# Performance work log

Hardware: AMD Instinct MI355X
Metric: run time of the kernel (lower is better)

The kernel has to match this reference:

```python
import jax, jax.numpy as jnp
import numpy as np

B, S, HID, NH = 2, 2048, 2048, 16
DH = HID // NH  # 128


def _rope_tables(seq_len, dim, dtype=jnp.float32):
    inv_freq = 1.0 / (10000.0 ** (jnp.arange(0, dim, 2, dtype=jnp.float32) / dim))
    t = jnp.arange(seq_len, dtype=jnp.float32)
    freqs = jnp.einsum('i,j->ij', t, inv_freq)          # [S, dim/2]
    emb = jnp.concatenate([freqs, freqs], axis=-1)       # [S, dim]
    return jnp.cos(emb)[None, None].astype(dtype), jnp.sin(emb)[None, None].astype(dtype)


def _rotate_half(x):
    x1, x2 = x[..., : x.shape[-1] // 2], x[..., x.shape[-1] // 2 :]
    return jnp.concatenate([-x2, x1], axis=-1)


def setup_inputs() -> dict:
    key = jax.random.key(0)
    ks = jax.random.split(key, 6)
    hidden_states = jax.random.normal(ks[0], (B, S, HID), dtype=jnp.float32)
    scale = 1.0 / np.sqrt(HID)
    Wq = jax.random.normal(ks[1], (HID, HID), dtype=jnp.float32) * scale
    Wk = jax.random.normal(ks[2], (HID, HID), dtype=jnp.float32) * scale
    Wv = jax.random.normal(ks[3], (HID, HID), dtype=jnp.float32) * scale
    Wo = jax.random.normal(ks[4], (HID, HID), dtype=jnp.float32) * scale
    bq = jnp.zeros((HID,), jnp.float32)
    bk = jnp.zeros((HID,), jnp.float32)
    bv = jnp.zeros((HID,), jnp.float32)
    bo = jnp.zeros((HID,), jnp.float32)
    # causal additive mask [1,1,S,S]
    causal = jnp.tril(jnp.ones((S, S), dtype=bool))
    attention_mask = jnp.where(causal, 0.0, -1e9).astype(jnp.float32)[None, None]
    return dict(hidden_states=hidden_states, attention_mask=attention_mask,
                Wq=Wq, bq=bq, Wk=Wk, bk=bk, Wv=Wv, bv=bv, Wo=Wo, bo=bo)


def reference(hidden_states, attention_mask, Wq, bq, Wk, bk, Wv, bv, Wo, bo):
    b, s, _ = hidden_states.shape
    # torch Linear: x @ W.T + b
    q = (hidden_states @ Wq.T + bq).reshape(b, s, NH, DH).transpose(0, 2, 1, 3)
    k = (hidden_states @ Wk.T + bk).reshape(b, s, NH, DH).transpose(0, 2, 1, 3)
    v = (hidden_states @ Wv.T + bv).reshape(b, s, NH, DH).transpose(0, 2, 1, 3)
    cos, sin = _rope_tables(s, DH)
    q = q * cos + _rotate_half(q) * sin
    k = k * cos + _rotate_half(k) * sin
    scores = jnp.einsum('bhqd,bhkd->bhqk', q * (DH ** -0.5), k)
    scores = scores + attention_mask
    probs = jax.nn.softmax(scores, axis=-1)  # dropout: eval mode (identity)
    out = jnp.einsum('bhqk,bhkd->bhqd', probs, v)
    out = out.transpose(0, 2, 1, 3).reshape(b, s, HID)
    return out @ Wo.T + bo
```

## Files before the change

kernel.cpp:

```cpp
#include <hip/hip_runtime.h>
#include <hip/hip_bf16.h>
#include <cstdint>
#include <cstddef>

#define BB 2
#define SS 2048
#define HH 2048
#define NHH 16
#define DHH 128

using f32x4  = __attribute__((ext_vector_type(4))) float;
using bf16x8 = __attribute__((ext_vector_type(8))) __bf16;
using bf16x4 = __attribute__((ext_vector_type(4))) __bf16;
using bfloat = __bf16;

__device__ inline void gload_lds16(const void* g, void* l) {
    __builtin_amdgcn_global_load_lds(
        (const __attribute__((address_space(1))) void*)g,
        (__attribute__((address_space(3))) void*)l, 16, 0, 0);
}

__device__ inline f32x4 mfma16(bf16x8 a, bf16x8 b, f32x4 c) {
    return __builtin_amdgcn_mfma_f32_16x16x32_bf16(a, b, c, 0, 0, 0);
}

template <int CTRL>
__device__ inline float dpp_max_step(float x) {
    int y = __builtin_amdgcn_update_dpp(0, __builtin_bit_cast(int, x), CTRL, 0xf, 0xf, false);
    return fmaxf(x, __builtin_bit_cast(float, y));
}
__device__ inline float rowmax16(float x) {
    x = dpp_max_step<0x121>(x);
    x = dpp_max_step<0x122>(x);
    x = dpp_max_step<0x124>(x);
    x = dpp_max_step<0x128>(x);
    return x;
}

__global__ void prep_all(const float* __restrict__ hs,
                         const float* __restrict__ w0, const float* __restrict__ w1,
                         const float* __restrict__ w2, const float* __restrict__ w3,
                         bfloat* __restrict__ xb,
                         bfloat* __restrict__ d0, bfloat* __restrict__ d1,
                         bfloat* __restrict__ d2, bfloat* __restrict__ d3,
                         float* __restrict__ cosT, float* __restrict__ sinT) {
    const int bid = blockIdx.x, tid = threadIdx.x;
    if (bid < 8192 + 16384) {
        const float* s;
        bfloat* d;
        int i;
        if (bid < 8192) {
            s = hs; d = xb; i = bid * 256 + tid;
        } else {
            int b2 = bid - 8192, sel = b2 >> 12;
            s = sel == 0 ? w0 : sel == 1 ? w1 : sel == 2 ? w2 : w3;
            d = sel == 0 ? d0 : sel == 1 ? d1 : sel == 2 ? d2 : d3;
            i = (b2 & 4095) * 256 + tid;
        }
        float4 v = reinterpret_cast<const float4*>(s)[i];
        bf16x4 o;
        o[0] = (bfloat)v.x; o[1] = (bfloat)v.y; o[2] = (bfloat)v.z; o[3] = (bfloat)v.w;
        reinterpret_cast<bf16x4*>(d)[i] = o;
    } else {
        int i = (bid - 24576) * 256 + tid;
        int s = i >> 6, j = i & 63;
        float invf = powf(10000.0f, -(float)j / 64.0f);
        float ang = (float)s * invf;
        cosT[i] = cosf(ang);
        sinT[i] = sinf(ang);
    }
}

__device__ __forceinline__ void kloop128(const bfloat* __restrict__ Ag,
                                         const bfloat* __restrict__ Bg,
                                         f32x4 (&acc)[4][4]) {
    constexpr int K = HH, NT = K / 32;
    __shared__ bfloat As[2][128 * 32];
    __shared__ bfloat Bs[2][128 * 32];
    const int t = threadIdx.x, l = t & 63, lr = l & 15, lg = l >> 4;
    const int w = t >> 6, wm = (w >> 1) * 64, wc = w & 1;
    const int ubase = t & ~63;

    auto stage = [&](int buf, int kt) {
#pragma unroll
        for (int i = 0; i < 2; i++) {
            int idx = i * 256 + t;
            int r = idx >> 2, u = idx & 3;
            int us = u ^ (r & 3) ^ ((r >> 2) & 1);
            gload_lds16(Ag + (size_t)r * K + kt * 32 + us * 8,
                        &As[buf][(i * 256 + ubase) * 8]);
        }
#pragma unroll
        for (int i = 0; i < 2; i++) {
            int idx = i * 256 + t;
            int r = idx >> 2, u = idx & 3;
            int us = u ^ (r & 3) ^ ((r >> 2) & 1);
            gload_lds16(Bg + (size_t)r * K + kt * 32 + us * 8,
                        &Bs[buf][(i * 256 + ubase) * 8]);
        }
    };

    stage(0, 0);

#pragma unroll 1
    for (int kt = 0; kt < NT; ++kt) {
        const int buf = kt & 1;
        asm volatile("s_waitcnt vmcnt(0)" ::: "memory");
        __builtin_amdgcn_s_barrier();
        __builtin_amdgcn_sched_barrier(0);
        if (kt + 1 < NT) stage(buf ^ 1, kt + 1);

        const bfloat* A_ = As[buf];
        const bfloat* B_ = Bs[buf];
        bf16x8 af[4], bfr[4];
#pragma unroll
        for (int mi = 0; mi < 4; mi++) {
            int row = wm + mi * 16 + lr;
            int us = lg ^ (row & 3) ^ ((row >> 2) & 1);
            af[mi] = *reinterpret_cast<const bf16x8*>(&A_[row * 32 + us * 8]);
        }
#pragma unroll
        for (int ni = 0; ni < 4; ni++) {
            int row = wc * 32 + (ni & 1) * 16 + (ni >> 1) * 64 + lr;
            int us = lg ^ (row & 3) ^ ((row >> 2) & 1);
            bfr[ni] = *reinterpret_cast<const bf16x8*>(&B_[row * 32 + us * 8]);
        }
        __builtin_amdgcn_s_setprio(1);
#pragma unroll
        for (int mi = 0; mi < 4; mi++)
#pragma unroll
            for (int ni = 0; ni < 4; ni++)
                acc[mi][ni] = mfma16(af[mi], bfr[ni], acc[mi][ni]);
        __builtin_amdgcn_s_setprio(0);
        __builtin_amdgcn_sched_barrier(0);
    }
}

__global__ __launch_bounds__(256, 4)
void gemm_qkv(const bfloat* __restrict__ A,
              const bfloat* __restrict__ Bq, const bfloat* __restrict__ Bk,
              const bfloat* __restrict__ Bv,
              const float* __restrict__ bq, const float* __restrict__ bk,
              const float* __restrict__ bv,
              bfloat* __restrict__ Qo, bfloat* __restrict__ Ko, bfloat* __restrict__ Vto,
              const float* __restrict__ cosT, const float* __restrict__ sinT) {
    constexpr int K = HH, N = HH;
    const int sel = blockIdx.y >> 4;
    const bfloat* Bt = sel == 0 ? Bq : sel == 1 ? Bk : Bv;
    const float* bias = sel == 0 ? bq : sel == 1 ? bk : bv;
    const int m0 = blockIdx.x * 128, n0 = (blockIdx.y & 15) * 128;

    f32x4 acc[4][4] = {};
    kloop128(A + (size_t)m0 * K, Bt + (size_t)n0 * K, acc);

    const int t = threadIdx.x, l = t & 63, lr = l & 15, lg = l >> 4;
    const int w = t >> 6, wm = (w >> 1) * 64, wc = w & 1;

    if (sel == 2) {
#pragma unroll
        for (int mi = 0; mi < 4; mi++) {
            int row = m0 + wm + mi * 16 + lg * 4;
            int bb = row >> 11;
            int s0 = row & (SS - 1);
#pragma unroll
            for (int ni = 0; ni < 4; ni++) {
                int cb = wc * 32 + (ni & 1) * 16 + (ni >> 1) * 64;
                int col = n0 + cb + lr;
                float bv_ = bias[col];
                bf16x4 pack;
#pragma unroll
                for (int j = 0; j < 4; j++)
                    pack[j] = (bfloat)(acc[mi][ni][j] + bv_);
                *reinterpret_cast<bf16x4*>(
                    &Vto[((size_t)(bb * HH + col)) * SS + s0]) = pack;
            }
        }
    } else {
        bfloat* C = sel == 0 ? Qo : Ko;
        const float qs = sel == 0 ? 0.088388347648318447f : 1.0f;
#pragma unroll
        for (int mi = 0; mi < 4; mi++) {
            int row = m0 + wm + mi * 16 + lg * 4;
#pragma unroll
            for (int ni = 0; ni < 2; ni++) {
                int d = wc * 32 + ni * 16 + lr;
                int col1 = n0 + d, col2 = col1 + 64;
                float b1 = bias[col1], b2 = bias[col2];
#pragma unroll
                for (int j = 0; j < 4; j++) {
                    int r = row + j, s = r & (SS - 1);
                    float c  = cosT[s * 64 + d];
                    float sn = sinT[s * 64 + d];
                    float x1 = acc[mi][ni][j] + b1;
                    float x2 = acc[mi][ni + 2][j] + b2;
                    C[(size_t)r * N + col1] = (bfloat)((x1 * c - x2 * sn) * qs);
                    C[(size_t)r * N + col2] = (bfloat)((x2 * c + x1 * sn) * qs);
                }
            }
        }
    }
}

__global__ __launch_bounds__(256, 4)
void gemm_out(const bfloat* __restrict__ A, const bfloat* __restrict__ Bt,
              const float* __restrict__ bias, float* __restrict__ C) {
    constexpr int K = HH, N = HH;
    const int m0 = blockIdx.x * 128, n0 = blockIdx.y * 128;

    f32x4 acc[4][4] = {};
    kloop128(A + (size_t)m0 * K, Bt + (size_t)n0 * K, acc);

    const int t = threadIdx.x, l = t & 63, lr = l & 15, lg = l >> 4;
    const int w = t >> 6, wm = (w >> 1) * 64, wc = w & 1;
#pragma unroll
    for (int mi = 0; mi < 4; mi++) {
        int row = m0 + wm + mi * 16 + lg * 4;
#pragma unroll
        for (int ni = 0; ni < 4; ni++) {
            int cb = wc * 32 + (ni & 1) * 16 + (ni >> 1) * 64;
            int col = n0 + cb + lr;
            float bv = bias[col];
#pragma unroll
            for (int j = 0; j < 4; j++)
                C[(size_t)(row + j) * N + col] = acc[mi][ni][j] + bv;
        }
    }
}

__global__ __launch_bounds__(256, 4)
void attn_fwd(const bfloat* __restrict__ Q, const bfloat* __restrict__ K,
              const bfloat* __restrict__ Vt, bfloat* __restrict__ O) {
    __shared__ bfloat Ks[64 * 128];
    __shared__ bfloat Vs[128 * 64];
    __shared__ bfloat Pw[4][16 * 64];

    const int t = threadIdx.x, w = t >> 6, l = t & 63;
    const int lr = l & 15, lg = l >> 4;
    const int swz = (lr & 7) << 4;

    const int f = blockIdx.x;
    const int xcd = f & 7, slot = f >> 3;
    const int bh = xcd + 8 * (slot >> 5);
    const int qidx = 31 - (slot & 31);
    const int b = bh >> 4, h = bh & 15;
    const int q0 = qidx * 64 + w * 16;

    const size_t bo_ = (size_t)b * SS * HH + (size_t)h * DHH;
    const bfloat* Qp = Q + bo_;
    const bfloat* Kp = K + bo_;
    const bfloat* Vp = Vt + (size_t)(b * NHH + h) * DHH * SS;
    bfloat* Op = O + bo_;

    auto stage = [&](int kv0) {
#pragma unroll
        for (int i = 0; i < 4; i++) {
            int Ub = (i * 4 + w) * 64;
            int U = Ub + l;
            int r = U >> 4;
            int u = (U & 15) ^ (r & 7);
            gload_lds16(Kp + (size_t)(kv0 + r) * HH + u * 8, &Ks[Ub * 8]);
        }
#pragma unroll
        for (int i = 0; i < 4; i++) {
            int Ub = (i * 4 + w) * 64;
            int U = Ub + l;
            int r = U >> 3;
            int u = (U & 7) ^ (r & 7);
            gload_lds16(Vp + (size_t)r * SS + kv0 + u * 8, &Vs[Ub * 8]);
        }
    };

    bf16x8 qf[4];
#pragma unroll
    for (int kt = 0; kt < 4; kt++)
        qf[kt] = *reinterpret_cast<const bf16x8*>(Qp + (size_t)(q0 + lr) * HH + kt * 32 + lg * 8);

    bf16x8 ones;
#pragma unroll
    for (int e = 0; e < 8; e++) ones[e] = (bfloat)1.0f;

    f32x4 o[8] = {};
    f32x4 lsv = {};
    float m[4];
#pragma unroll
    for (int j = 0; j < 4; j++) m[j] = -1e30f;

    const int nkv = qidx + 1;

    for (int kv = 0; kv < nkv; ++kv) {
        stage(kv * 64);
        __syncthreads();

        const char* KB = (const char*)&Ks[0];
        const char* VB = (const char*)&Vs[0];

        f32x4 sc[4] = {};
        __builtin_amdgcn_s_setprio(1);
#pragma unroll
        for (int kt = 0; kt < 4; kt++) {
            const int col = (kt * 64 + lg * 16);
#pragma unroll
            for (int kb = 0; kb < 4; kb++) {
                bf16x8 kf = *reinterpret_cast<const bf16x8*>(
                    KB + (kb * 16 + lr) * 256 + (col ^ swz));
                sc[kb] = mfma16(qf[kt], kf, sc[kb]);
            }
        }
        __builtin_amdgcn_s_setprio(0);

        const bool diag = (kv == nkv - 1);
        float p[4][4], alpha[4];
        bool ga = false;
#pragma unroll
        for (int j = 0; j < 4; j++) {
            float v0 = sc[0][j], v1 = sc[1][j], v2 = sc[2][j], v3 = sc[3][j];
            if (diag) {
                int qr = q0 + lg * 4 + j;
                int k0 = kv * 64 + lr;
                if (k0      > qr) v0 = -1e30f;
                if (k0 + 16 > qr) v1 = -1e30f;
                if (k0 + 32 > qr) v2 = -1e30f;
                if (k0 + 48 > qr) v3 = -1e30f;
            }
            float mx = rowmax16(fmaxf(fmaxf(v0, v1), fmaxf(v2, v3)));
            bool grow = mx > m[j] + 8.0f;
            float mn = grow ? mx : m[j];
            alpha[j] = grow ? __expf(m[j] - mn) : 1.0f;
            m[j] = mn;
            ga = ga || grow;
            p[0][j] = __expf(v0 - mn);
            p[1][j] = __expf(v1 - mn);
            p[2][j] = __expf(v2 - mn);
            p[3][j] = __expf(v3 - mn);
        }
        if (__any(ga)) {
#pragma unroll
            for (int j = 0; j < 4; j++) {
                lsv[j] *= alpha[j];
#pragma unroll
                for (int nt = 0; nt < 8; nt++) o[nt][j] *= alpha[j];
            }
        }

        char* pwb = (char*)&Pw[w][0];
#pragma unroll
        for (int j = 0; j < 4; j++) {
            int q = lg * 4 + j;
            int qs = (q & 7) << 4;
#pragma unroll
            for (int kb = 0; kb < 4; kb++)
                *(bfloat*)(pwb + q * 128 + ((kb * 32 + lr * 2) ^ qs)) = (bfloat)p[kb][j];
        }
        asm volatile("s_waitcnt lgkmcnt(0)" ::: "memory");
        __builtin_amdgcn_sched_barrier(0);

        const char* pwr = (const char*)&Pw[w][0];
        bf16x8 pa0 = *reinterpret_cast<const bf16x8*>(pwr + lr * 128 + ((lg * 16) ^ swz));
        bf16x8 pa1 = *reinterpret_cast<const bf16x8*>(pwr + lr * 128 + ((64 + lg * 16) ^ swz));
        __builtin_amdgcn_s_setprio(1);
        lsv = mfma16(pa0, ones, lsv);
        lsv = mfma16(pa1, ones, lsv);
#pragma unroll
        for (int nt = 0; nt < 8; nt++) {
            const char* vb = VB + (nt * 16 + lr) * 128;
            bf16x8 vf0 = *reinterpret_cast<const bf16x8*>(vb + ((lg * 16) ^ swz));
            bf16x8 vf1 = *reinterpret_cast<const bf16x8*>(vb + ((64 + lg * 16) ^ swz));
            o[nt] = mfma16(pa0, vf0, o[nt]);
            o[nt] = mfma16(pa1, vf1, o[nt]);
        }
        __builtin_amdgcn_s_setprio(0);
        __syncthreads();
    }

#pragma unroll
    for (int j = 0; j < 4; j++) {
        float inv = 1.0f / lsv[j];
        int row = q0 + lg * 4 + j;
#pragma unroll
        for (int nt = 0; nt < 8; nt++)
            Op[(size_t)row * HH + nt * 16 + lr] = (bfloat)(o[nt][j] * inv);
    }
}

extern "C" void kernel_launch(void* const* d_in, const int* in_sizes, int n_in,
                              void* d_out, int out_size, void* d_ws, size_t ws_size,
                              hipStream_t stream) {
    (void)in_sizes; (void)n_in; (void)out_size; (void)ws_size;
    const float* hs = (const float*)d_in[0];
    const float* Wq = (const float*)d_in[2];
    const float* bq = (const float*)d_in[3];
    const float* Wk = (const float*)d_in[4];
    const float* bk = (const float*)d_in[5];
    const float* Wv = (const float*)d_in[6];
    const float* bv = (const float*)d_in[7];
    const float* Wo = (const float*)d_in[8];
    const float* bo = (const float*)d_in[9];

    char* ws = (char*)d_ws;
    size_t off = 0;
    auto alloc = [&](size_t bytes) { void* p = ws + off; off += (bytes + 255) & ~(size_t)255; return p; };
    const size_t MK = (size_t)BB * SS * HH;
    const size_t NK = (size_t)HH * HH;

    bfloat* Xb  = (bfloat*)alloc(MK * 2);
    bfloat* Wqb = (bfloat*)alloc(NK * 2);
    bfloat* Wkb = (bfloat*)alloc(NK * 2);
    bfloat* Wvb = (bfloat*)alloc(NK * 2);
    bfloat* Wob = (bfloat*)alloc(NK * 2);
    bfloat* Qb  = (bfloat*)alloc(MK * 2);
    bfloat* Kb  = (bfloat*)alloc(MK * 2);
    bfloat* Vtb = (bfloat*)alloc(MK * 2);
    float*  cosT = (float*)alloc((size_t)SS * 64 * 4);
    float*  sinT = (float*)alloc((size_t)SS * 64 * 4);
    bfloat* AOb = Xb;

    prep_all<<<8192 + 16384 + 512, 256, 0, stream>>>(
        hs, Wq, Wk, Wv, Wo, Xb, Wqb, Wkb, Wvb, Wob, cosT, sinT);

    gemm_qkv<<<dim3(32, 48), 256, 0, stream>>>(
        Xb, Wqb, Wkb, Wvb, bq, bk, bv, Qb, Kb, Vtb, cosT, sinT);

    attn_fwd<<<1024, 256, 0, stream>>>(Qb, Kb, Vtb, AOb);

    gemm_out<<<dim3(32, 16), 256, 0, stream>>>(AOb, Wob, bo, (float*)d_out);
}
```

Baseline: 307.6 us.

## Pair causal query tiles per block and double-buffer K/V staging in attention

Each attention block now handles two 64-row query tiles, qa and 31-qa, from the same head. This balances causal work across blocks, and each staged K/V tile serves both query tiles, halving the grid. K/V staging uses two LDS buffers, so the next tile's global-to-LDS load is issued before computing on the current one, replacing the per-iteration full sync pattern. The cost is more registers (two sets of accumulators and Q fragments) and double the LDS. Launch bounds drop from 4 to 2 blocks per CU, which reduces occupancy.

```diff
diff --git a/kernel.cpp b/kernel.cpp
--- a/kernel.cpp
+++ b/kernel.cpp
@@ -227,11 +227,11 @@
     }
 }
 
-__global__ __launch_bounds__(256, 4)
+__global__ __launch_bounds__(256, 2)
 void attn_fwd(const bfloat* __restrict__ Q, const bfloat* __restrict__ K,
               const bfloat* __restrict__ Vt, bfloat* __restrict__ O) {
-    __shared__ bfloat Ks[64 * 128];
-    __shared__ bfloat Vs[128 * 64];
+    __shared__ bfloat Ks[2][64 * 128];
+    __shared__ bfloat Vs[2][128 * 64];
     __shared__ bfloat Pw[4][16 * 64];
 
     const int t = threadIdx.x, w = t >> 6, l = t & 63;
@@ -239,11 +239,10 @@
     const int swz = (lr & 7) << 4;
 
     const int f = blockIdx.x;
-    const int xcd = f & 7, slot = f >> 3;
-    const int bh = xcd + 8 * (slot >> 5);
-    const int qidx = 31 - (slot & 31);
+    const int bh = f & 31, p = f >> 5;
+    const int qa = p, qb = 31 - p;
     const int b = bh >> 4, h = bh & 15;
-    const int q0 = qidx * 64 + w * 16;
+    const int q0a = qa * 64 + w * 16, q0b = qb * 64 + w * 16;
 
     const size_t bo_ = (size_t)b * SS * HH + (size_t)h * DHH;
     const bfloat* Qp = Q + bo_;
@@ -251,14 +250,14 @@
     const bfloat* Vp = Vt + (size_t)(b * NHH + h) * DHH * SS;
     bfloat* Op = O + bo_;
 
-    auto stage = [&](int kv0) {
+    auto stage = [&](int buf, int kv0) {
 #pragma unroll
         for (int i = 0; i < 4; i++) {
             int Ub = (i * 4 + w) * 64;
             int U = Ub + l;
             int r = U >> 4;
             int u = (U & 15) ^ (r & 7);
-            gload_lds16(Kp + (size_t)(kv0 + r) * HH + u * 8, &Ks[Ub * 8]);
+            gload_lds16(Kp + (size_t)(kv0 + r) * HH + u * 8, &Ks[buf][Ub * 8]);
         }
 #pragma unroll
         for (int i = 0; i < 4; i++) {
@@ -266,34 +265,29 @@
             int U = Ub + l;
             int r = U >> 3;
             int u = (U & 7) ^ (r & 7);
-            gload_lds16(Vp + (size_t)r * SS + kv0 + u * 8, &Vs[Ub * 8]);
+            gload_lds16(Vp + (size_t)r * SS + kv0 + u * 8, &Vs[buf][Ub * 8]);
         }
     };
 
-    bf16x8 qf[4];
-#pragma unroll
-    for (int kt = 0; kt < 4; kt++)
-        qf[kt] = *reinterpret_cast<const bf16x8*>(Qp + (size_t)(q0 + lr) * HH + kt * 32 + lg * 8);
+    bf16x8 qfA[4], qfB[4];
+#pragma unroll
+    for (int kt = 0; kt < 4; kt++) {
+        qfA[kt] = *reinterpret_cast<const bf16x8*>(Qp + (size_t)(q0a + lr) * HH + kt * 32 + lg * 8);
+        qfB[kt] = *reinterpret_cast<const bf16x8*>(Qp + (size_t)(q0b + lr) * HH + kt * 32 + lg * 8);
+    }
 
     bf16x8 ones;
 #pragma unroll
     for (int e = 0; e < 8; e++) ones[e] = (bfloat)1.0f;
 
-    f32x4 o[8] = {};
-    f32x4 lsv = {};
-    float m[4];
-#pragma unroll
-    for (int j = 0; j < 4; j++) m[j] = -1e30f;
-
-    const int nkv = qidx + 1;
-
-    for (int kv = 0; kv < nkv; ++kv) {
-        stage(kv * 64);
-        __syncthreads();
-
-        const char* KB = (const char*)&Ks[0];
-        const char* VB = (const char*)&Vs[0];
-
+    f32x4 oA[8] = {}, oB[8] = {};
+    f32x4 lsvA = {}, lsvB = {};
+    float mA[4], mB[4];
+#pragma unroll
+    for (int j = 0; j < 4; j++) { mA[j] = -1e30f; mB[j] = -1e30f; }
+
+    auto process = [&](bf16x8 (&qf)[4], f32x4 (&o)[8], f32x4& lsv, float (&m)[4],
+                       int q0, int kv, bool diag, const char* KB, const char* VB) {
         f32x4 sc[4] = {};
         __builtin_amdgcn_s_setprio(1);
 #pragma unroll
@@ -308,8 +302,7 @@
         }
         __builtin_amdgcn_s_setprio(0);
 
-        const bool diag = (kv == nkv - 1);
-        float p[4][4], alpha[4];
+        float pv[4][4], alpha[4];
         bool ga = false;
 #pragma unroll
         for (int j = 0; j < 4; j++) {
@@ -328,10 +321,10 @@
             alpha[j] = grow ? __expf(m[j] - mn) : 1.0f;
             m[j] = mn;
             ga = ga || grow;
-            p[0][j] = __expf(v0 - mn);
-            p[1][j] = __expf(v1 - mn);
-            p[2][j] = __expf(v2 - mn);
-            p[3][j] = __expf(v3 - mn);
+            pv[0][j] = __expf(v0 - mn);
+            pv[1][j] = __expf(v1 - mn);
+            pv[2][j] = __expf(v2 - mn);
+            pv[3][j] = __expf(v3 - mn);
         }
         if (__any(ga)) {
 #pragma unroll
@@ -349,7 +342,7 @@
             int qs = (q & 7) << 4;
 #pragma unroll
             for (int kb = 0; kb < 4; kb++)
-                *(bfloat*)(pwb + q * 128 + ((kb * 32 + lr * 2) ^ qs)) = (bfloat)p[kb][j];
+                *(bfloat*)(pwb + q * 128 + ((kb * 32 + lr * 2) ^ qs)) = (bfloat)pv[kb][j];
         }
         asm volatile("s_waitcnt lgkmcnt(0)" ::: "memory");
         __builtin_amdgcn_sched_barrier(0);
@@ -369,17 +362,39 @@
             o[nt] = mfma16(pa1, vf1, o[nt]);
         }
         __builtin_amdgcn_s_setprio(0);
-        __syncthreads();
-    }
-
-#pragma unroll
-    for (int j = 0; j < 4; j++) {
-        float inv = 1.0f / lsv[j];
-        int row = q0 + lg * 4 + j;
-#pragma unroll
-        for (int nt = 0; nt < 8; nt++)
-            Op[(size_t)row * HH + nt * 16 + lr] = (bfloat)(o[nt][j] * inv);
-    }
+    };
+
+    const int nkv = qb + 1;
+    stage(0, 0);
+
+#pragma unroll 1
+    for (int kv = 0; kv < nkv; ++kv) {
+        const int buf = kv & 1;
+        asm volatile("s_waitcnt vmcnt(0)" ::: "memory");
+        __builtin_amdgcn_s_barrier();
+        __builtin_amdgcn_sched_barrier(0);
+        if (kv + 1 < nkv) stage(buf ^ 1, (kv + 1) * 64);
+
+        const char* KB = (const char*)&Ks[buf][0];
+        const char* VB = (const char*)&Vs[buf][0];
+
+        process(qfB, oB, lsvB, mB, q0b, kv, kv == qb, KB, VB);
+        if (kv <= qa)
+            process(qfA, oA, lsvA, mA, q0a, kv, kv == qa, KB, VB);
+    }
+
+    auto epi = [&](f32x4 (&o)[8], f32x4& lsv, int q0) {
+#pragma unroll
+        for (int j = 0; j < 4; j++) {
+            float inv = 1.0f / lsv[j];
+            int row = q0 + lg * 4 + j;
+#pragma unroll
+            for (int nt = 0; nt < 8; nt++)
+                Op[(size_t)row * HH + nt * 16 + lr] = (bfloat)(o[nt][j] * inv);
+        }
+    };
+    epi(oB, lsvB, q0b);
+    epi(oA, lsvA, q0a);
 }
 
 extern "C" void kernel_launch(void* const* d_in, const int* in_sizes, int n_in,
@@ -420,7 +435,7 @@
     gemm_qkv<<<dim3(32, 48), 256, 0, stream>>>(
         Xb, Wqb, Wkb, Wvb, bq, bk, bv, Qb, Kb, Vtb, cosT, sinT);
 
-    attn_fwd<<<1024, 256, 0, stream>>>(Qb, Kb, Vtb, AOb);
+    attn_fwd<<<512, 256, 0, stream>>>(Qb, Kb, Vtb, AOb);
 
     gemm_out<<<dim3(32, 16), 256, 0, stream>>>(AOb, Wob, bo, (float*)d_out);
 }
```

After: 272.7 us, median of 2. 11.4% less time.
